# Optimization experiments

Measured on AMD Instinct MI355X. Metric: run time of the kernel, lower is better.

Reference implementation:

```python
import jax, jax.numpy as jnp
import numpy as np

N, E, F_IN, H, D, HID, G = 50000, 800000, 64, 4, 32, 128, 1024
NEG_SLOPE = 0.2


def setup_inputs():
    key = jax.random.key(0)
    ks = jax.random.split(key, 32)
    inp = {
        "x": jax.random.normal(ks[0], (N, F_IN), dtype=jnp.float32),
        "edge_index": jax.random.randint(ks[1], (2, E), 0, N, dtype=jnp.int64),
        "batch": jnp.sort(jax.random.randint(ks[2], (N,), 0, G, dtype=jnp.int64)),
    }
    dims = [F_IN, HID, HID]
    i = 3
    for l, din in enumerate(dims):
        s = 1.0 / np.sqrt(din)
        inp[f"Wl{l}"] = jax.random.normal(ks[i], (din, H * D), dtype=jnp.float32) * s; i += 1
        inp[f"bl{l}"] = jnp.zeros((H * D,), dtype=jnp.float32)
        inp[f"Wr{l}"] = jax.random.normal(ks[i], (din, H * D), dtype=jnp.float32) * s; i += 1
        inp[f"br{l}"] = jnp.zeros((H * D,), dtype=jnp.float32)
        inp[f"att{l}"] = jax.random.normal(ks[i], (H, D), dtype=jnp.float32) * (1.0 / np.sqrt(D)); i += 1
        inp[f"b{l}"] = jnp.zeros((H * D,), dtype=jnp.float32)
    inp["Wh"] = jax.random.normal(ks[i], (HID, 1), dtype=jnp.float32) * (1.0 / np.sqrt(HID))
    inp["bh"] = jnp.zeros((1,), dtype=jnp.float32)
    return inp


def gatv2_layer(x, src, dst, Wl, bl, Wr, br, att, b):
    # GATv2Conv (eval mode, no dropout): e_ij = att . leaky_relu(Wl x_j + Wr x_i)
    xl = (x @ Wl + bl).reshape(-1, H, D)   # source transform
    xr = (x @ Wr + br).reshape(-1, H, D)   # target transform
    m = xl[src] + xr[dst]                  # [E,H,D]
    e = jnp.where(m >= 0, m, NEG_SLOPE * m)
    score = jnp.einsum("ehd,hd->eh", e, att)          # [E,H]
    smax = jax.ops.segment_max(score, dst, num_segments=N)  # [N,H]
    expv = jnp.exp(score - smax[dst])
    denom = jax.ops.segment_sum(expv, dst, num_segments=N)
    alpha = expv / denom[dst]                          # softmax over in-edges of dst
    agg = jax.ops.segment_sum(alpha[:, :, None] * xl[src], dst, num_segments=N)
    return agg.reshape(-1, H * D) + b


def reference(x, edge_index, batch, Wl0, bl0, Wr0, br0, att0, b0,
              Wl1, bl1, Wr1, br1, att1, b1,
              Wl2, bl2, Wr2, br2, att2, b2, Wh, bh):
    src, dst = edge_index[0], edge_index[1]
    params = [(Wl0, bl0, Wr0, br0, att0, b0),
              (Wl1, bl1, Wr1, br1, att1, b1),
              (Wl2, bl2, Wr2, br2, att2, b2)]
    h = x
    for p in params:
        h = gatv2_layer(h, src, dst, *p)
        h = jax.nn.elu(h)  # dropout inactive in eval
    # global mean pool over graphs
    sums = jax.ops.segment_sum(h, batch, num_segments=G)
    cnt = jax.ops.segment_sum(jnp.ones((h.shape[0],), h.dtype), batch, num_segments=G)
    pooled = sums / jnp.maximum(cnt, 1.0)[:, None]
    return pooled @ Wh + bh
```

## Files before the change

kernel.cpp:

```cpp
#include <hip/hip_runtime.h>
#include <math.h>

#define N_NODES 50000
#define N_EDGES 800000
#define HD 128
#define GG 1024
#define NEG_SLOPE 0.2f
#define SCAN_B 1024
#define NB ((N_NODES + SCAN_B - 1) / SCAN_B)
#define NXCONV (N_NODES * 64)
#define NWCONV 81920

typedef __attribute__((ext_vector_type(8))) short bf16x8;
typedef __attribute__((ext_vector_type(4))) float f32x4;
typedef __attribute__((ext_vector_type(2))) float f32x2;

__device__ __forceinline__ unsigned short f2bf(float v) {
    unsigned u = __float_as_uint(v);
    u += 0x7fff + ((u >> 16) & 1);
    return (unsigned short)(u >> 16);
}
__device__ __forceinline__ float bf2f(unsigned short s) {
    return __uint_as_float((unsigned)s << 16);
}

__global__ void convert_prep(const float* __restrict__ x,
                             unsigned short* __restrict__ Xh, unsigned short* __restrict__ Xl,
                             const float* __restrict__ W0l, const float* __restrict__ W0r,
                             const float* __restrict__ W1l, const float* __restrict__ W1r,
                             const float* __restrict__ W2l, const float* __restrict__ W2r,
                             unsigned short* __restrict__ Wth, unsigned short* __restrict__ Wtl,
                             const int* __restrict__ dst, int* __restrict__ deg,
                             const int* __restrict__ batch, int* __restrict__ gptr)
{
    const int i = blockIdx.x * 256 + threadIdx.x;
    if (i < NXCONV) {
        const float v = x[i];
        const unsigned short hi = f2bf(v);
        Xh[i] = hi;
        Xl[i] = f2bf(v - bf2f(hi));
        return;
    }
    if (i < NXCONV + NWCONV) {
        const int t = i - NXCONV;
        const float* Wl; const float* Wr;
        int c, k, o;
        if (t < 16384) {
            c = t >> 6; k = t & 63; o = t;
            Wl = W0l; Wr = W0r;
        } else if (t < 49152) {
            const int b = t - 16384; c = b >> 7; k = b & 127; o = 32768 + b;
            Wl = W1l; Wr = W1r;
        } else {
            const int b = t - 49152; c = b >> 7; k = b & 127; o = 65536 + b;
            Wl = W2l; Wr = W2r;
        }
        const float v = (c < 128) ? Wl[(size_t)k * 128 + c] : Wr[(size_t)k * 128 + (c - 128)];
        const unsigned short hi = f2bf(v);
        Wth[o] = hi;
        Wtl[o] = f2bf(v - bf2f(hi));
        return;
    }
    const int e = i - NXCONV - NWCONV;
    if (e < N_EDGES) atomicAdd(&deg[dst[e]], 1);
    if (e > N_NODES) return;
    if (e == 0) {
        for (int g = 0; g <= batch[0]; g++) gptr[g] = 0;
    } else if (e == N_NODES) {
        for (int g = batch[N_NODES - 1] + 1; g <= GG; g++) gptr[g] = N_NODES;
    } else {
        const int b0 = batch[e - 1], b1 = batch[e];
        for (int g = b0 + 1; g <= b1; g++) gptr[g] = e;
    }
}

__launch_bounds__(SCAN_B)
__global__ void scan_block(const int* __restrict__ deg, int* __restrict__ rowptr,
                           int* __restrict__ btot)
{
    __shared__ int s[SCAN_B];
    const int tid = threadIdx.x;
    const int i = blockIdx.x * SCAN_B + tid;
    int v = (i < N_NODES) ? deg[i] : 0;
    s[tid] = v;
    __syncthreads();
    for (int off = 1; off < SCAN_B; off <<= 1) {
        int t = (tid >= off) ? s[tid - off] : 0;
        __syncthreads();
        s[tid] += t;
        __syncthreads();
    }
    if (i < N_NODES) rowptr[i] = s[tid] - v;
    if (tid == SCAN_B - 1) btot[blockIdx.x] = s[SCAN_B - 1];
}

__launch_bounds__(256)
__global__ void scan_add(const int* __restrict__ btot, int* __restrict__ rowptr,
                         int* __restrict__ cursor)
{
    __shared__ int sb[NB + 1];
    const int tid = threadIdx.x;
    if (tid < 64) {
        const int v = (tid < NB) ? btot[tid] : 0;
        int incl = v;
        #pragma unroll
        for (int off = 1; off < 64; off <<= 1) {
            const int t = __shfl_up(incl, off);
            if (tid >= off) incl += t;
        }
        if (tid < NB) sb[tid] = incl - v;
        if (tid == NB - 1) sb[NB] = incl;
    }
    __syncthreads();
    const int i = blockIdx.x * 256 + tid;
    if (i < N_NODES) {
        const int r = rowptr[i] + sb[i >> 10];
        rowptr[i] = r;
        cursor[i] = r;
    }
    if (i == N_NODES) rowptr[N_NODES] = sb[NB];
}

__global__ void scatter_csr(const int* __restrict__ src, const int* __restrict__ dst,
                            int* __restrict__ cursor, int* __restrict__ csr_src)
{
    int e = blockIdx.x * 256 + threadIdx.x;
    if (e >= N_EDGES) return;
    int pos = atomicAdd(&cursor[dst[e]], 1);
    csr_src[pos] = src[e];
}

template<int K>
__launch_bounds__(256, 3)
__global__ void gemm_lds(const unsigned short* __restrict__ Xh, const unsigned short* __restrict__ Xl,
                         const unsigned short* __restrict__ Wth, const unsigned short* __restrict__ Wtl,
                         const float* __restrict__ bl, const float* __restrict__ br,
                         float* __restrict__ Cl, float* __restrict__ Cr, int n)
{
    constexpr int NCH = K / 32;
    constexpr int STR = K + 8;
    constexpr int RT  = (N_NODES + 63) / 64;
    __shared__ unsigned short AsH[64 * STR], AsL[64 * STR];
    const int tid  = threadIdx.x;
    const int wave = tid >> 6;
    const int lane = tid & 63;
    const int quad = lane >> 4;
    const int l15  = lane & 15;
    const int cg   = blockIdx.x & 1;
    const int rs   = blockIdx.x >> 1;
    const int NS   = gridDim.x >> 1;
    const int colid = cg * 4 + wave;
    const int cb32  = colid * 32;

    bf16x8 Bh[NCH][2], Bo[NCH][2];
    #pragma unroll
    for (int ch = 0; ch < NCH; ch++)
        #pragma unroll
        for (int nt = 0; nt < 2; nt++) {
            const size_t wo = (size_t)(cb32 + nt * 16 + l15) * K + ch * 32 + quad * 8;
            Bh[ch][nt] = *(const bf16x8*)(Wth + wo);
            Bo[ch][nt] = *(const bf16x8*)(Wtl + wo);
        }

    const int cb = cb32 & 127;
    const float* bias = (colid < 4) ? bl : br;
    float* C = (colid < 4) ? Cl : Cr;
    const float bv0 = bias[cb + l15];
    const float bv1 = bias[cb + 16 + l15];

    for (int rt = rs; rt < RT; rt += NS) {
        const int row0 = rt * 64;
        {
            constexpr int THR = K / 8;
            constexpr int RPP = 256 / THR;
            const int sr = tid / THR, seg = tid % THR;
            #pragma unroll
            for (int ps = 0; ps < 64 / RPP; ps++) {
                const int r = ps * RPP + sr;
                int gr = row0 + r;
                gr = (gr < n) ? gr : (n - 1);
                const size_t go = (size_t)gr * K + seg * 8;
                *(uint4*)&AsH[r * STR + seg * 8] = *(const uint4*)(Xh + go);
                *(uint4*)&AsL[r * STR + seg * 8] = *(const uint4*)(Xl + go);
            }
        }
        __syncthreads();

        f32x4 acc[4][2];
        #pragma unroll
        for (int mt = 0; mt < 4; mt++) {
            acc[mt][0] = (f32x4){0.f, 0.f, 0.f, 0.f};
            acc[mt][1] = (f32x4){0.f, 0.f, 0.f, 0.f};
        }
        #pragma unroll
        for (int ch = 0; ch < NCH; ch++) {
            bf16x8 ah[4], al[4];
            #pragma unroll
            for (int mt = 0; mt < 4; mt++) {
                ah[mt] = *(const bf16x8*)&AsH[(mt * 16 + l15) * STR + ch * 32 + quad * 8];
                al[mt] = *(const bf16x8*)&AsL[(mt * 16 + l15) * STR + ch * 32 + quad * 8];
            }
            #pragma unroll
            for (int nt = 0; nt < 2; nt++)
                #pragma unroll
                for (int mt = 0; mt < 4; mt++) {
                    acc[mt][nt] = __builtin_amdgcn_mfma_f32_16x16x32_bf16(ah[mt], Bh[ch][nt], acc[mt][nt], 0, 0, 0);
                    acc[mt][nt] = __builtin_amdgcn_mfma_f32_16x16x32_bf16(ah[mt], Bo[ch][nt], acc[mt][nt], 0, 0, 0);
                    acc[mt][nt] = __builtin_amdgcn_mfma_f32_16x16x32_bf16(al[mt], Bh[ch][nt], acc[mt][nt], 0, 0, 0);
                }
        }

        #pragma unroll
        for (int nt = 0; nt < 2; nt++) {
            const float bv = nt ? bv1 : bv0;
            #pragma unroll
            for (int mt = 0; mt < 4; mt++)
                #pragma unroll
                for (int r = 0; r < 4; r++) {
                    const int row = row0 + mt * 16 + quad * 4 + r;
                    if (row < n)
                        C[(size_t)row * 128 + cb + nt * 16 + l15] = acc[mt][nt][r] + bv;
                }
        }
        __syncthreads();
    }
}

template<int LAST>
__launch_bounds__(256)
__global__ void node_attn(const float* __restrict__ xl, const float* __restrict__ xr,
                          const int* __restrict__ rowptr, const int* __restrict__ csr_src,
                          const float* __restrict__ att, const float* __restrict__ bvec,
                          unsigned short* __restrict__ Hh, unsigned short* __restrict__ Hl,
                          const float* __restrict__ Wh, float* __restrict__ pernode)
{
    const int node = (blockIdx.x * 256 + threadIdx.x) >> 6;
    const int lane = threadIdx.x & 63;
    if (node >= N_NODES) return;
    const int grp = lane >> 4;
    const int li  = lane & 15;

    const size_t nb = (size_t)node * HD + li * 8;
    f32x2 xrp[4], awp[4];
    {
        const float4 a = *(const float4*)(xr + nb);
        const float4 b = *(const float4*)(xr + nb + 4);
        xrp[0] = (f32x2){a.x, a.y}; xrp[1] = (f32x2){a.z, a.w};
        xrp[2] = (f32x2){b.x, b.y}; xrp[3] = (f32x2){b.z, b.w};
        const float4 c = *(const float4*)(att + li * 8);
        const float4 d = *(const float4*)(att + li * 8 + 4);
        awp[0] = (f32x2){c.x, c.y}; awp[1] = (f32x2){c.z, c.w};
        awp[2] = (f32x2){d.x, d.y}; awp[3] = (f32x2){d.z, d.w};
    }
    const f32x2 nsl = (f32x2){NEG_SLOPE, NEG_SLOPE};
    const int beg = rowptr[node];
    const int end = rowptr[node + 1];

    float m = -1e30f, l = 0.f;
    f32x2 accp[4];
    #pragma unroll
    for (int j = 0; j < 4; j++) accp[j] = (f32x2){0.f, 0.f};

    f32x2 vp[4];
    {
        const int e0 = beg + grp;
        const int s0 = (e0 < end) ? csr_src[e0] : 0;
        const float4 a = *(const float4*)(xl + (size_t)s0 * HD + li * 8);
        const float4 b = *(const float4*)(xl + (size_t)s0 * HD + li * 8 + 4);
        vp[0] = (f32x2){a.x, a.y}; vp[1] = (f32x2){a.z, a.w};
        vp[2] = (f32x2){b.x, b.y}; vp[3] = (f32x2){b.z, b.w};
    }

    for (int base = beg; base < end; base += 4) {
        const bool valid = (base + grp) < end;
        f32x2 np[4];
        #pragma unroll
        for (int j = 0; j < 4; j++) np[j] = vp[j];
        if (base + 4 < end) {
            const int e2 = base + 4 + grp;
            const int s2 = (e2 < end) ? csr_src[e2] : 0;
            const float4 a = *(const float4*)(xl + (size_t)s2 * HD + li * 8);
            const float4 b = *(const float4*)(xl + (size_t)s2 * HD + li * 8 + 4);
            np[0] = (f32x2){a.x, a.y}; np[1] = (f32x2){a.z, a.w};
            np[2] = (f32x2){b.x, b.y}; np[3] = (f32x2){b.z, b.w};
        }
        f32x2 pd0 = (f32x2){0.f, 0.f}, pd1 = (f32x2){0.f, 0.f};
        #pragma unroll
        for (int j = 0; j < 4; j++) {
            f32x2 t = vp[j] + xrp[j];
            const f32x2 u = t * nsl;
            t[0] = fmaxf(t[0], u[0]);
            t[1] = fmaxf(t[1], u[1]);
            if (j & 1) pd1 = t * awp[j] + pd1;
            else       pd0 = t * awp[j] + pd0;
        }
        const f32x2 pds = pd0 + pd1;
        float p = pds[0] + pds[1];
        p += __shfl_xor(p, 1);
        p += __shfl_xor(p, 2);

        const float mn = valid ? fmaxf(m, p) : m;
        const float w  = valid ? __expf(p - mn) : 0.f;
        const float sc = __expf(m - mn);
        l = fmaf(l, sc, w);
        const f32x2 w2  = (f32x2){w, w};
        const f32x2 sc2 = (f32x2){sc, sc};
        #pragma unroll
        for (int j = 0; j < 4; j++) {
            accp[j] = accp[j] * sc2 + w2 * vp[j];
            vp[j] = np[j];
        }
        m = mn;
    }

    #pragma unroll
    for (int off = 16; off < 64; off <<= 1) {
        const float mo = __shfl_xor(m, off);
        const float lo = __shfl_xor(l, off);
        f32x2 bo[4];
        #pragma unroll
        for (int j = 0; j < 4; j++) {
            bo[j][0] = __shfl_xor(accp[j][0], off);
            bo[j][1] = __shfl_xor(accp[j][1], off);
        }
        const float mm = fmaxf(m, mo);
        const float e1 = __expf(m - mm);
        const float e2 = __expf(mo - mm);
        l = l * e1 + lo * e2;
        const f32x2 e1p = (f32x2){e1, e1};
        const f32x2 e2p = (f32x2){e2, e2};
        #pragma unroll
        for (int j = 0; j < 4; j++)
            accp[j] = accp[j] * e1p + bo[j] * e2p;
        m = mm;
    }

    if (grp == 0) {
        const float inv = (l > 0.f) ? 1.f / l : 0.f;
        const float4 bb0 = *(const float4*)(bvec + li * 8);
        const float4 bb1 = *(const float4*)(bvec + li * 8 + 4);
        float o[8];
        o[0] = fmaf(accp[0][0], inv, bb0.x);
        o[1] = fmaf(accp[0][1], inv, bb0.y);
        o[2] = fmaf(accp[1][0], inv, bb0.z);
        o[3] = fmaf(accp[1][1], inv, bb0.w);
        o[4] = fmaf(accp[2][0], inv, bb1.x);
        o[5] = fmaf(accp[2][1], inv, bb1.y);
        o[6] = fmaf(accp[3][0], inv, bb1.z);
        o[7] = fmaf(accp[3][1], inv, bb1.w);
        #pragma unroll
        for (int j = 0; j < 8; j++)
            o[j] = (o[j] > 0.f) ? o[j] : expm1f(o[j]);
        if (LAST) {
            const float4 w0 = *(const float4*)(Wh + li * 8);
            const float4 w1 = *(const float4*)(Wh + li * 8 + 4);
            float da = o[0] * w0.x + o[2] * w0.z;
            float db = o[1] * w0.y + o[3] * w0.w;
            da = fmaf(o[4], w1.x, da); db = fmaf(o[5], w1.y, db);
            da = fmaf(o[6], w1.z, da); db = fmaf(o[7], w1.w, db);
            float d = da + db;
            d += __shfl_xor(d, 1);
            d += __shfl_xor(d, 2);
            d += __shfl_xor(d, 4);
            d += __shfl_xor(d, 8);
            if (li == 0) pernode[node] = d;
        } else {
            bf16x8 hv, lv;
            #pragma unroll
            for (int j = 0; j < 8; j++) {
                unsigned short h = f2bf(o[j]);
                hv[j] = (short)h;
                lv[j] = (short)f2bf(o[j] - bf2f(h));
            }
            *(bf16x8*)(Hh + nb) = hv;
            *(bf16x8*)(Hl + nb) = lv;
        }
    }
}

__launch_bounds__(256)
__global__ void finish_head(const float* __restrict__ pernode, const int* __restrict__ gptr,
                            const float* __restrict__ bh, float* __restrict__ out)
{
    const int g = (blockIdx.x * 256 + threadIdx.x) >> 6;
    const int lane = threadIdx.x & 63;
    if (g >= GG) return;
    const int b0 = gptr[g], b1 = gptr[g + 1];
    float s = 0.f;
    for (int i = b0 + lane; i < b1; i += 64) s += pernode[i];
    s += __shfl_xor(s, 1);
    s += __shfl_xor(s, 2);
    s += __shfl_xor(s, 4);
    s += __shfl_xor(s, 8);
    s += __shfl_xor(s, 16);
    s += __shfl_xor(s, 32);
    if (lane == 0) out[g] = s / fmaxf((float)(b1 - b0), 1.f) + bh[0];
}

extern "C" void kernel_launch(void* const* d_in, const int* in_sizes, int n_in,
                              void* d_out, int out_size, void* d_ws, size_t ws_size,
                              hipStream_t stream)
{
    const float* x     = (const float*)d_in[0];
    const int*   edge  = (const int*)d_in[1];
    const int*   batch = (const int*)d_in[2];
    const int*   src   = edge;
    const int*   dst   = edge + N_EDGES;
    const float* Wh    = (const float*)d_in[21];
    const float* bh    = (const float*)d_in[22];
    float* out = (float*)d_out;

    const size_t N128 = (size_t)N_NODES * HD;
    float* buf_xl = (float*)d_ws;
    float* buf_xr = buf_xl + N128;
    unsigned short* Xh  = (unsigned short*)(buf_xr + N128);
    unsigned short* Xl_ = Xh + N128;
    unsigned short* Wth = Xl_ + N128;
    unsigned short* Wtl = Wth + 3 * 256 * 128;
    int* deg       = (int*)(Wtl + 3 * 256 * 128);
    float* pernode = (float*)(deg + N_NODES);
    int* rowptr  = (int*)(pernode + N_NODES);
    int* cursor  = rowptr + N_NODES + 1;
    int* csr_src = cursor + N_NODES;
    int* btot    = csr_src + N_EDGES;
    int* gptr    = btot + NB;

    hipMemsetAsync(deg, 0, (size_t)N_NODES * sizeof(int), stream);
    convert_prep<<<(NXCONV + NWCONV + N_EDGES + 255) / 256, 256, 0, stream>>>(
        x, Xh, Xl_,
        (const float*)d_in[3], (const float*)d_in[5],
        (const float*)d_in[9], (const float*)d_in[11],
        (const float*)d_in[15], (const float*)d_in[17],
        Wth, Wtl, dst, deg, batch, gptr);
    scan_block<<<NB, SCAN_B, 0, stream>>>(deg, rowptr, btot);
    scan_add<<<(N_NODES + 256) / 256, 256, 0, stream>>>(btot, rowptr, cursor);
    scatter_csr<<<(N_EDGES + 255) / 256, 256, 0, stream>>>(src, dst, cursor, csr_src);

    const int gemm_grid = 768;
    const int attn_grid = (N_NODES + 3) / 4;

    for (int l = 0; l < 3; l++) {
        const float* bl  = (const float*)d_in[4 + 6 * l];
        const float* br  = (const float*)d_in[6 + 6 * l];
        const float* att = (const float*)d_in[7 + 6 * l];
        const float* bb  = (const float*)d_in[8 + 6 * l];

        if (l == 0)
            gemm_lds<64><<<gemm_grid, 256, 0, stream>>>(Xh, Xl_, Wth, Wtl,
                                                        bl, br, buf_xl, buf_xr, N_NODES);
        else
            gemm_lds<128><<<gemm_grid, 256, 0, stream>>>(Xh, Xl_,
                                                         Wth + l * 256 * 128, Wtl + l * 256 * 128,
                                                         bl, br, buf_xl, buf_xr, N_NODES);
        if (l < 2)
            node_attn<0><<<attn_grid, 256, 0, stream>>>(buf_xl, buf_xr, rowptr, csr_src,
                                                        att, bb, Xh, Xl_,
                                                        nullptr, nullptr);
        else
            node_attn<1><<<attn_grid, 256, 0, stream>>>(buf_xl, buf_xr, rowptr, csr_src,
                                                        att, bb, nullptr, nullptr,
                                                        Wh, pernode);
    }

    finish_head<<<GG / 4, 256, 0, stream>>>(pernode, gptr, bh, out);
}
```

Baseline: 447.0 us.

## Use 512-thread GEMM blocks with register-prefetched A tiles and vectorized x conversion

Each GEMM block now has 8 waves covering all 256 output columns (left and right weights), so each A tile is loaded into LDS once per block instead of twice across two blocks. The next row tile is prefetched into registers while the MFMA work runs on the current tile, then written to LDS after a barrier. The grid drops to 256 persistent blocks. The x bf16 split conversion now processes float4 per thread. The trade-off is higher register pressure from the prefetch buffers and fewer blocks to hide latency.

```diff
diff --git a/kernel.cpp b/kernel.cpp
--- a/kernel.cpp
+++ b/kernel.cpp
@@ -8,7 +8,7 @@
 #define NEG_SLOPE 0.2f
 #define SCAN_B 1024
 #define NB ((N_NODES + SCAN_B - 1) / SCAN_B)
-#define NXCONV (N_NODES * 64)
+#define NXV4 800000
 #define NWCONV 81920
 
 typedef __attribute__((ext_vector_type(8))) short bf16x8;
@@ -34,15 +34,19 @@
                              const int* __restrict__ batch, int* __restrict__ gptr)
 {
     const int i = blockIdx.x * 256 + threadIdx.x;
-    if (i < NXCONV) {
-        const float v = x[i];
-        const unsigned short hi = f2bf(v);
-        Xh[i] = hi;
-        Xl[i] = f2bf(v - bf2f(hi));
+    if (i < NXV4) {
+        const float4 v = *(const float4*)(x + (size_t)i * 4);
+        ushort4 h, lo;
+        h.x = f2bf(v.x); lo.x = f2bf(v.x - bf2f(h.x));
+        h.y = f2bf(v.y); lo.y = f2bf(v.y - bf2f(h.y));
+        h.z = f2bf(v.z); lo.z = f2bf(v.z - bf2f(h.z));
+        h.w = f2bf(v.w); lo.w = f2bf(v.w - bf2f(h.w));
+        *(ushort4*)(Xh + (size_t)i * 4) = h;
+        *(ushort4*)(Xl + (size_t)i * 4) = lo;
         return;
     }
-    if (i < NXCONV + NWCONV) {
-        const int t = i - NXCONV;
+    if (i < NXV4 + NWCONV) {
+        const int t = i - NXV4;
         const float* Wl; const float* Wr;
         int c, k, o;
         if (t < 16384) {
@@ -61,7 +65,7 @@
         Wtl[o] = f2bf(v - bf2f(hi));
         return;
     }
-    const int e = i - NXCONV - NWCONV;
+    const int e = i - NXV4 - NWCONV;
     if (e < N_EDGES) atomicAdd(&deg[dst[e]], 1);
     if (e > N_NODES) return;
     if (e == 0) {
@@ -131,7 +135,7 @@
 }
 
 template<int K>
-__launch_bounds__(256, 3)
+__launch_bounds__(512, 2)
 __global__ void gemm_lds(const unsigned short* __restrict__ Xh, const unsigned short* __restrict__ Xl,
                          const unsigned short* __restrict__ Wth, const unsigned short* __restrict__ Wtl,
                          const float* __restrict__ bl, const float* __restrict__ br,
@@ -140,17 +144,17 @@
     constexpr int NCH = K / 32;
     constexpr int STR = K + 8;
     constexpr int RT  = (N_NODES + 63) / 64;
+    constexpr int THR = K / 8;
+    constexpr int RPP = 512 / THR;
+    constexpr int NPASS = 64 / RPP;
     __shared__ unsigned short AsH[64 * STR], AsL[64 * STR];
     const int tid  = threadIdx.x;
     const int wave = tid >> 6;
     const int lane = tid & 63;
     const int quad = lane >> 4;
     const int l15  = lane & 15;
-    const int cg   = blockIdx.x & 1;
-    const int rs   = blockIdx.x >> 1;
-    const int NS   = gridDim.x >> 1;
-    const int colid = cg * 4 + wave;
-    const int cb32  = colid * 32;
+    const int cb32 = wave * 32;
+    const int sr   = tid / THR, seg = tid % THR;
 
     bf16x8 Bh[NCH][2], Bo[NCH][2];
     #pragma unroll
@@ -163,29 +167,48 @@
         }
 
     const int cb = cb32 & 127;
-    const float* bias = (colid < 4) ? bl : br;
-    float* C = (colid < 4) ? Cl : Cr;
+    const float* bias = (wave < 4) ? bl : br;
+    float* C = (wave < 4) ? Cl : Cr;
     const float bv0 = bias[cb + l15];
     const float bv1 = bias[cb + 16 + l15];
 
-    for (int rt = rs; rt < RT; rt += NS) {
-        const int row0 = rt * 64;
-        {
-            constexpr int THR = K / 8;
-            constexpr int RPP = 256 / THR;
-            const int sr = tid / THR, seg = tid % THR;
-            #pragma unroll
-            for (int ps = 0; ps < 64 / RPP; ps++) {
-                const int r = ps * RPP + sr;
-                int gr = row0 + r;
+    uint4 rh[NPASS], rl[NPASS];
+    {
+        const int rt = blockIdx.x;
+        #pragma unroll
+        for (int p = 0; p < NPASS; p++) {
+            const int r = p * RPP + sr;
+            int gr = rt * 64 + r;
+            gr = (gr < n) ? gr : (n - 1);
+            const size_t go = (size_t)gr * K + seg * 8;
+            rh[p] = *(const uint4*)(Xh + go);
+            rl[p] = *(const uint4*)(Xl + go);
+        }
+        #pragma unroll
+        for (int p = 0; p < NPASS; p++) {
+            const int r = p * RPP + sr;
+            *(uint4*)&AsH[r * STR + seg * 8] = rh[p];
+            *(uint4*)&AsL[r * STR + seg * 8] = rl[p];
+        }
+    }
+    __syncthreads();
+
+    const int NS = gridDim.x;
+    for (int rt = blockIdx.x; rt < RT; rt += NS) {
+        const int rtn = rt + NS;
+        if (rtn < RT) {
+            #pragma unroll
+            for (int p = 0; p < NPASS; p++) {
+                const int r = p * RPP + sr;
+                int gr = rtn * 64 + r;
                 gr = (gr < n) ? gr : (n - 1);
                 const size_t go = (size_t)gr * K + seg * 8;
-                *(uint4*)&AsH[r * STR + seg * 8] = *(const uint4*)(Xh + go);
-                *(uint4*)&AsL[r * STR + seg * 8] = *(const uint4*)(Xl + go);
+                rh[p] = *(const uint4*)(Xh + go);
+                rl[p] = *(const uint4*)(Xl + go);
             }
         }
-        __syncthreads();
-
+
+        const int row0 = rt * 64;
         f32x4 acc[4][2];
         #pragma unroll
         for (int mt = 0; mt < 4; mt++) {
@@ -221,6 +244,16 @@
                     if (row < n)
                         C[(size_t)row * 128 + cb + nt * 16 + l15] = acc[mt][nt][r] + bv;
                 }
+        }
+
+        __syncthreads();
+        if (rtn < RT) {
+            #pragma unroll
+            for (int p = 0; p < NPASS; p++) {
+                const int r = p * RPP + sr;
+                *(uint4*)&AsH[r * STR + seg * 8] = rh[p];
+                *(uint4*)&AsL[r * STR + seg * 8] = rl[p];
+            }
         }
         __syncthreads();
     }
@@ -426,7 +459,7 @@
     int* gptr    = btot + NB;
 
     hipMemsetAsync(deg, 0, (size_t)N_NODES * sizeof(int), stream);
-    convert_prep<<<(NXCONV + NWCONV + N_EDGES + 255) / 256, 256, 0, stream>>>(
+    convert_prep<<<(NXV4 + NWCONV + N_EDGES + 256) / 256, 256, 0, stream>>>(
         x, Xh, Xl_,
         (const float*)d_in[3], (const float*)d_in[5],
         (const float*)d_in[9], (const float*)d_in[11],
@@ -436,7 +469,7 @@
     scan_add<<<(N_NODES + 256) / 256, 256, 0, stream>>>(btot, rowptr, cursor);
     scatter_csr<<<(N_EDGES + 255) / 256, 256, 0, stream>>>(src, dst, cursor, csr_src);
 
-    const int gemm_grid = 768;
+    const int gemm_grid = 256;
     const int attn_grid = (N_NODES + 3) / 4;
 
     for (int l = 0; l < 3; l++) {
@@ -446,10 +479,10 @@
         const float* bb  = (const float*)d_in[8 + 6 * l];
 
         if (l == 0)
-            gemm_lds<64><<<gemm_grid, 256, 0, stream>>>(Xh, Xl_, Wth, Wtl,
+            gemm_lds<64><<<gemm_grid, 512, 0, stream>>>(Xh, Xl_, Wth, Wtl,
                                                         bl, br, buf_xl, buf_xr, N_NODES);
         else
-            gemm_lds<128><<<gemm_grid, 256, 0, stream>>>(Xh, Xl_,
+            gemm_lds<128><<<gemm_grid, 512, 0, stream>>>(Xh, Xl_,
                                                          Wth + l * 256 * 128, Wtl + l * 256 * 128,
                                                          bl, br, buf_xl, buf_xr, N_NODES);
         if (l < 2)
```

Measured after the change: 463.5 us. 3.7% more time.
